# Optimization experiments

Hardware: AMD Instinct MI355X
Metric: run time of the kernel (lower is better)

## Reference

```python
import jax, jax.numpy as jnp
import numpy as np

B, L, D = 4, 512, 768          # batch, seq, d_model
NL, DI, N, K, R = 12, 1536, 16, 4, 48  # layers, d_inner, d_state, d_conv, dt_rank
V, P = 50257, 1024             # vocab, positions
EPS = 1e-5


def setup_inputs() -> dict:
    key = jax.random.key(0)
    ks = jax.random.split(key, 12)
    p = lambda i, shape, s=0.02: jax.random.normal(ks[i], shape, jnp.float32) * s
    return {
        "input_ids": jax.random.randint(ks[0], (B, L), 0, V),
        "wte": p(1, (V, D)),
        "wpe": p(2, (P, D)),
        "ln_g": jnp.ones((NL, D), jnp.float32),
        "ln_b": jnp.zeros((NL, D), jnp.float32),
        "in_W": p(3, (NL, 2 * DI, D)),
        "conv_W": p(4, (NL, DI, K), 0.2),
        "conv_b": jnp.zeros((NL, DI), jnp.float32),
        "xp_W": p(5, (NL, R + 2 * N, DI)),
        "dt_W": p(6, (NL, DI, R), 0.1),
        "dt_b": p(7, (NL, DI), 0.5),
        # Mamba S4D-real init: A = -exp(A_log), A_log = log(1..N)
        "A_log": jnp.tile(jnp.log(jnp.arange(1, N + 1, dtype=jnp.float32)), (NL, DI, 1)),
        "Dres": jnp.ones((NL, DI), jnp.float32),
        "out_W": p(8, (NL, D, DI)),
        "nf_g": jnp.ones((D,), jnp.float32),
        "nf_b": jnp.zeros((D,), jnp.float32),
        "fin_g": jnp.ones((D,), jnp.float32),
        "fin_b": jnp.zeros((D,), jnp.float32),
    }


def layer_norm(x, g, b):
    mu = jnp.mean(x, -1, keepdims=True)
    var = jnp.mean((x - mu) ** 2, -1, keepdims=True)
    return (x - mu) * jax.lax.rsqrt(var + EPS) * g + b


def causal_conv(x, w, b):
    # x: (B, L, DI); depthwise causal conv, kernel K, left pad K-1, truncate to L
    xt = jnp.transpose(x, (0, 2, 1))  # (B, DI, L)
    y = jax.lax.conv_general_dilated(
        xt, w[:, None, :], (1,), [(K - 1, 0)],
        feature_group_count=DI, dimension_numbers=("NCH", "OIH", "NCH"))
    return jnp.transpose(y + b[None, :, None], (0, 2, 1))


def selective_scan(u, delta, A, Bm, Cm):
    # u, delta: (B, L, DI); A: (DI, N); Bm, Cm: (B, L, N)
    def step(h, inp):
        u_t, d_t, b_t, c_t = inp  # (B,DI), (B,DI), (B,N), (B,N)
        dA = jnp.exp(d_t[:, :, None] * A)            # (B, DI, N)
        h = h * dA + (d_t * u_t)[:, :, None] * b_t[:, None, :]
        y = jnp.einsum("bdn,bn->bd", h, c_t)
        return h, y

    h0 = jnp.zeros((u.shape[0], DI, N), u.dtype)
    xs = (jnp.swapaxes(u, 0, 1), jnp.swapaxes(delta, 0, 1),
          jnp.swapaxes(Bm, 0, 1), jnp.swapaxes(Cm, 0, 1))
    _, ys = jax.lax.scan(step, h0, xs)               # ys: (L, B, DI)
    return jnp.swapaxes(ys, 0, 1)


def mamba_mixer(x, inW, cW, cb, xpW, dtW, dtb, a_log, dres, outW):
    xz = jnp.einsum("bld,ed->ble", x, inW)           # (B, L, 2*DI)
    xi, z = jnp.split(xz, 2, axis=-1)
    xi = jax.nn.silu(causal_conv(xi, cW, cb))
    dbl = jnp.einsum("bld,ed->ble", xi, xpW)         # (B, L, R+2N)
    dt, Bm, Cm = dbl[..., :R], dbl[..., R:R + N], dbl[..., R + N:]
    delta = jax.nn.softplus(jnp.einsum("blr,dr->bld", dt, dtW) + dtb)
    A = -jnp.exp(a_log)
    y = selective_scan(xi, delta, A, Bm, Cm) + xi * dres
    y = y * jax.nn.silu(z)
    return jnp.einsum("ble,de->bld", y, outW)


def reference(input_ids, wte, wpe, ln_g, ln_b, in_W, conv_W, conv_b, xp_W,
              dt_W, dt_b, A_log, Dres, out_W, nf_g, nf_b, fin_g, fin_b):
    emb = wte[input_ids] + wpe[: input_ids.shape[1]]  # (B, L, D); dropout=identity (eval)
    hidden, residual = emb, None
    for i in range(NL):
        residual = hidden if residual is None else hidden + residual
        h = layer_norm(residual, ln_g[i], ln_b[i])
        hidden = mamba_mixer(h, in_W[i], conv_W[i], conv_b[i], xp_W[i],
                             dt_W[i], dt_b[i], A_log[i], Dres[i], out_W[i])
    residual = hidden + residual
    out = layer_norm(residual, nf_g, nf_b)   # MixerModel.norm_f
    return layer_norm(out, fin_g, fin_b)     # decoder self.norm
```

## Files before the change

### kernel.cpp

```cpp
#include <hip/hip_runtime.h>

#define BB 4
#define LL 512
#define DD 768
#define NLAYER 12
#define DI 1536
#define NS 16
#define KC 4
#define RR 48
#define MROWS (BB*LL)
#define E2 (2*DI)
#define EPSV 1e-5f
#define CH2 16
#define LC2 (LL/CH2)
#define LOG2E 1.4426950408889634f
#define XPZ 12

typedef __attribute__((ext_vector_type(8))) short bf16x8;
typedef __attribute__((ext_vector_type(4))) float f32x4;

#define GLL16(g, l) __builtin_amdgcn_global_load_lds( \
    (const __attribute__((address_space(1))) void*)(g), \
    (__attribute__((address_space(3))) void*)(l), 16, 0, 0)

__device__ inline float hw_exp2(float x) { return __builtin_amdgcn_exp2f(x); }

__device__ inline ushort f2bf(float f) {
  union { float f; unsigned u; } v; v.f = f;
  unsigned u = v.u;
  unsigned r = (u + 0x7fffu + ((u >> 16) & 1u)) >> 16;
  return (ushort)r;
}
__device__ inline float bf2f(ushort u) {
  union { unsigned u; float f; } v; v.u = ((unsigned)u) << 16; return v.f;
}

__device__ inline float block_sum(float v, volatile float* red) {
  #pragma unroll
  for (int o = 32; o > 0; o >>= 1) v += __shfl_down(v, o);
  if ((threadIdx.x & 63) == 0) red[threadIdx.x >> 6] = v;
  __syncthreads();
  float t = red[0] + red[1] + red[2] + red[3];
  __syncthreads();
  return t;
}

__global__ __launch_bounds__(256) void k_cvtA(const float* __restrict__ inW,
    const float* __restrict__ outW, ushort* __restrict__ wIn,
    ushort* __restrict__ wOut) {
  int i = blockIdx.x * 256 + threadIdx.x;
  const int nIn = NLAYER * E2 * DD / 4;
  const int nOut = NLAYER * DD * DI / 4;
  if (i < nIn) {
    float4 v = ((const float4*)inW)[i];
    ushort4 o = { f2bf(v.x), f2bf(v.y), f2bf(v.z), f2bf(v.w) };
    ((ushort4*)wIn)[i] = o;
  } else if (i < nIn + nOut) {
    int j = i - nIn;
    float4 v = ((const float4*)outW)[j];
    ushort4 o = { f2bf(v.x), f2bf(v.y), f2bf(v.z), f2bf(v.w) };
    ((ushort4*)wOut)[j] = o;
  }
}

__global__ __launch_bounds__(256) void k_cvtB(const float* __restrict__ xpW,
    const float* __restrict__ dtW, const float* __restrict__ convW,
    ushort* __restrict__ wXp, ushort* __restrict__ wDt, float* __restrict__ convWt) {
  int i = blockIdx.x * 256 + threadIdx.x;
  const int n0 = NLAYER * 80 * DI / 4;
  const int n1 = NLAYER * DI * 64;
  const int n2 = NLAYER * DI * 4;
  if (i < n0) {
    float4 v = ((const float4*)xpW)[i];
    ushort4 o = { f2bf(v.x), f2bf(v.y), f2bf(v.z), f2bf(v.w) };
    ((ushort4*)wXp)[i] = o;
  } else if (i < n0 + n1) {
    int j = i - n0;
    int r = j >> 6, c = j & 63;
    wDt[j] = (c < RR) ? f2bf(dtW[(size_t)r * RR + c]) : (ushort)0;
  } else if (i < n0 + n1 + n2) {
    int j = i - n0 - n1;
    int l = j / (DI * 4);
    int rem = j - l * (DI * 4);
    int d = rem >> 2, k = rem & 3;
    convWt[(size_t)l * 4 * DI + k * DI + d] = convW[(size_t)l * DI * 4 + d * 4 + k];
  }
}

__global__ __launch_bounds__(256) void k_embed(const int* __restrict__ ids,
    const float* __restrict__ wte, const float* __restrict__ wpe,
    float* __restrict__ resid) {
  const int nd4 = DD / 4;
  int i = blockIdx.x * 256 + threadIdx.x;
  if (i >= MROWS * nd4) return;
  int m = i / nd4, d4 = i - m * nd4;
  int l = m & (LL - 1);
  int tok = ids[m];
  float4 a = ((const float4*)wte)[(size_t)tok * nd4 + d4];
  float4 b = ((const float4*)wpe)[(size_t)l * nd4 + d4];
  float4 o; o.x = a.x + b.x; o.y = a.y + b.y; o.z = a.z + b.z; o.w = a.w + b.w;
  ((float4*)resid)[i] = o;
}

__global__ __launch_bounds__(256) void k_ln(const float* __restrict__ h0,
    const float* __restrict__ h1,
    float* __restrict__ resid, const float* __restrict__ g, const float* __restrict__ b,
    ushort* __restrict__ hbf, int addHidden) {
  __shared__ float red[4];
  int m = blockIdx.x, t = threadIdx.x;
  size_t base = (size_t)m * DD;
  float x0 = resid[base + t], x1 = resid[base + t + 256], x2 = resid[base + t + 512];
  if (addHidden) {
    x0 += h0[base + t]       + h1[base + t];
    x1 += h0[base + t + 256] + h1[base + t + 256];
    x2 += h0[base + t + 512] + h1[base + t + 512];
    resid[base + t] = x0; resid[base + t + 256] = x1; resid[base + t + 512] = x2;
  }
  float S  = block_sum(x0 + x1 + x2, red);
  float S2 = block_sum(x0*x0 + x1*x1 + x2*x2, red);
  float mu = S * (1.f / DD);
  float var = S2 * (1.f / DD) - mu * mu;
  float rs = rsqrtf(var + EPSV);
  hbf[base + t]       = f2bf((x0 - mu) * rs * g[t]       + b[t]);
  hbf[base + t + 256] = f2bf((x1 - mu) * rs * g[t + 256] + b[t + 256]);
  hbf[base + t + 512] = f2bf((x2 - mu) * rs * g[t + 512] + b[t + 512]);
}

template<int OM>
__global__ __launch_bounds__(256) void k_gemm64(const ushort* __restrict__ A,
    const ushort* __restrict__ Bw, void* __restrict__ Cv, const float* __restrict__ dtb,
    int N, int K, int kSteps) {
  __shared__ ushort lA[64 * 64];
  __shared__ ushort lB[128 * 64];
  int tid = threadIdx.x;
  int wid = tid >> 6, lane = tid & 63;
  int tm = blockIdx.y * 64, tn = blockIdx.x * 128;
  int kBase = blockIdx.z * kSteps * 64;
  int wr = (wid >> 1) * 32, wc = (wid & 1) * 64;
  int fr = lane & 15, kg = lane >> 4;
  int sR = lane >> 3;
  int sC = ((lane & 7) ^ sR) * 8;
  f32x4 acc[2][4];
  #pragma unroll
  for (int mi = 0; mi < 2; ++mi)
    #pragma unroll
    for (int ni = 0; ni < 4; ++ni)
      acc[mi][ni] = {0.f, 0.f, 0.f, 0.f};

  for (int ks = 0; ks < kSteps; ++ks) {
    int k0 = kBase + ks * 64;
    #pragma unroll
    for (int i = 0; i < 2; ++i) {
      int r0 = wid * 16 + i * 8;
      GLL16(A + (size_t)(tm + r0 + sR) * K + k0 + sC, &lA[r0 * 64]);
    }
    #pragma unroll
    for (int i = 0; i < 4; ++i) {
      int r0 = wid * 32 + i * 8;
      int brow = tn + r0 + sR;
      if (brow > N - 1) brow = N - 1;
      GLL16(Bw + (size_t)brow * K + k0 + sC, &lB[r0 * 64]);
    }
    __syncthreads();
    #pragma unroll
    for (int k2 = 0; k2 < 2; ++k2) {
      bf16x8 af[2], bfr[4];
      #pragma unroll
      for (int mi = 0; mi < 2; ++mi)
        af[mi] = *(const bf16x8*)&lA[(wr + mi * 16 + fr) * 64 + (((k2 * 4 + kg) ^ (fr & 7)) * 8)];
      #pragma unroll
      for (int ni = 0; ni < 4; ++ni)
        bfr[ni] = *(const bf16x8*)&lB[(wc + ni * 16 + fr) * 64 + (((k2 * 4 + kg) ^ (fr & 7)) * 8)];
      #pragma unroll
      for (int mi = 0; mi < 2; ++mi)
        #pragma unroll
        for (int ni = 0; ni < 4; ++ni)
          acc[mi][ni] = __builtin_amdgcn_mfma_f32_16x16x32_bf16(af[mi], bfr[ni], acc[mi][ni], 0, 0, 0);
    }
    __syncthreads();
  }
  int crow0 = tm + wr + kg * 4;
  int ccol0 = tn + wc + fr;
  if (OM == 0) {
    float* C = (float*)Cv + (size_t)blockIdx.z * ((size_t)gridDim.y * 64) * N;
    #pragma unroll
    for (int mi = 0; mi < 2; ++mi)
      #pragma unroll
      for (int ni = 0; ni < 4; ++ni) {
        int cc = ccol0 + ni * 16;
        if (cc < N) {
          #pragma unroll
          for (int j = 0; j < 4; ++j)
            C[(size_t)(crow0 + mi * 16 + j) * N + cc] = acc[mi][ni][j];
        }
      }
  } else if (OM == 1) {
    ushort* C = (ushort*)Cv;
    #pragma unroll
    for (int mi = 0; mi < 2; ++mi)
      #pragma unroll
      for (int ni = 0; ni < 4; ++ni) {
        int cc = ccol0 + ni * 16;
        if (cc < N) {
          #pragma unroll
          for (int j = 0; j < 4; ++j)
            C[(size_t)(crow0 + mi * 16 + j) * N + cc] = f2bf(acc[mi][ni][j]);
        }
      }
  } else {
    float* C = (float*)Cv;
    #pragma unroll
    for (int mi = 0; mi < 2; ++mi)
      #pragma unroll
      for (int ni = 0; ni < 4; ++ni) {
        int cc = ccol0 + ni * 16;
        if (cc < N) {
          float bv = dtb[cc];
          #pragma unroll
          for (int j = 0; j < 4; ++j) {
            float x = acc[mi][ni][j] + bv;
            float sp = (x > 20.f) ? x : log1pf(__expf(x));
            C[(size_t)(crow0 + mi * 16 + j) * N + cc] = sp;
          }
        }
      }
  }
}

__global__ __launch_bounds__(256) void k_xpconv(const ushort* __restrict__ xz,
    const ushort* __restrict__ wXpL, const float* __restrict__ cwt,
    const float* __restrict__ cbl, ushort* __restrict__ xibf,
    float* __restrict__ xpPart) {
  __shared__ ushort lA[64 * 64];
  __shared__ ushort lB[128 * 64];
  int tid = threadIdx.x;
  int wid = tid >> 6, lane = tid & 63;
  int tm2 = blockIdx.y * 64;
  int kBase = blockIdx.z * 128;
  int wr = (wid >> 1) * 32, wc = (wid & 1) * 64;
  int fr = lane & 15, kg = lane >> 4;
  int sR = lane >> 3, sC = ((lane & 7) ^ sR) * 8;
  f32x4 acc[2][4];
  #pragma unroll
  for (int mi = 0; mi < 2; ++mi)
    #pragma unroll
    for (int ni = 0; ni < 4; ++ni)
      acc[mi][ni] = {0.f, 0.f, 0.f, 0.f};
  for (int ks = 0; ks < 2; ++ks) {
    int k0 = kBase + ks * 64;
    #pragma unroll
    for (int i2 = 0; i2 < 4; ++i2) {
      int r0 = wid * 32 + i2 * 8;
      int brow = r0 + sR;
      if (brow > 79) brow = 79;
      GLL16(wXpL + (size_t)brow * DI + k0 + sC, &lB[r0 * 64]);
    }
    #pragma unroll
    for (int c2 = 0; c2 < 2; ++c2) {
      int chunk = tid + c2 * 256;
      int row = chunk >> 3, cc8 = chunk & 7;
      int m = tm2 + row, l = m & (LL - 1);
      int gc = k0 + cc8 * 8;
      float a8[8];
      {
        float4 a = *(const float4*)&cbl[gc];
        float4 b = *(const float4*)&cbl[gc + 4];
        a8[0] = a.x; a8[1] = a.y; a8[2] = a.z; a8[3] = a.w;
        a8[4] = b.x; a8[5] = b.y; a8[6] = b.z; a8[7] = b.w;
      }
      #pragma unroll
      for (int t = 0; t < 4; ++t) {
        if (l - 3 + t >= 0) {
          float4 a = *(const float4*)&cwt[t * DI + gc];
          float4 b = *(const float4*)&cwt[t * DI + gc + 4];
          bf16x8 v = *(const bf16x8*)&xz[(size_t)(m - 3 + t) * E2 + gc];
          a8[0] += bf2f((ushort)v[0]) * a.x; a8[1] += bf2f((ushort)v[1]) * a.y;
          a8[2] += bf2f((ushort)v[2]) * a.z; a8[3] += bf2f((ushort)v[3]) * a.w;
          a8[4] += bf2f((ushort)v[4]) * b.x; a8[5] += bf2f((ushort)v[5]) * b.y;
          a8[6] += bf2f((ushort)v[6]) * b.z; a8[7] += bf2f((ushort)v[7]) * b.w;
        }
      }
      bf16x8 vo;
      #pragma unroll
      for (int j = 0; j < 8; ++j) {
        float sg = 1.f / (1.f + __expf(-a8[j]));
        vo[j] = (short)f2bf(a8[j] * sg);
      }
      *(bf16x8*)&lA[row * 64 + ((cc8 ^ (row & 7)) * 8)] = vo;
      *(bf16x8*)&xibf[(size_t)m * DI + gc] = vo;
    }
    __syncthreads();
    #pragma unroll
    for (int k2 = 0; k2 < 2; ++k2) {
      bf16x8 af[2], bf4[4];
      #pragma unroll
      for (int mi = 0; mi < 2; ++mi)
        af[mi] = *(const bf16x8*)&lA[(wr + mi * 16 + fr) * 64 + (((k2 * 4 + kg) ^ (fr & 7)) * 8)];
      #pragma unroll
      for (int ni = 0; ni < 4; ++ni)
        bf4[ni] = *(const bf16x8*)&lB[(wc + ni * 16 + fr) * 64 + (((k2 * 4 + kg) ^ (fr & 7)) * 8)];
      #pragma unroll
      for (int mi = 0; mi < 2; ++mi)
        #pragma unroll
        for (int ni = 0; ni < 4; ++ni)
          acc[mi][ni] = __builtin_amdgcn_mfma_f32_16x16x32_bf16(af[mi], bf4[ni], acc[mi][ni], 0, 0, 0);
    }
    __syncthreads();
  }
  int crow0 = tm2 + wr + kg * 4;
  int ccol0 = wc + fr;
  float* Cf = xpPart + (size_t)blockIdx.z * MROWS * 80;
  #pragma unroll
  for (int mi = 0; mi < 2; ++mi)
    #pragma unroll
    for (int ni = 0; ni < 4; ++ni) {
      int cc = ccol0 + ni * 16;
      if (cc < 80) {
        #pragma unroll
        for (int j = 0; j < 4; ++j)
          Cf[(size_t)(crow0 + mi * 16 + j) * 80 + cc] = acc[mi][ni][j];
      }
    }
}

__global__ __launch_bounds__(256) void k_comb_xp(const float* __restrict__ part,
    float* __restrict__ dblb, ushort* __restrict__ dtbf) {
  int i = blockIdx.x * 256 + threadIdx.x;
  if (i >= MROWS * 80) return;
  const int S = MROWS * 80;
  float s = 0.f;
  #pragma unroll
  for (int z = 0; z < XPZ; ++z) s += part[i + z * S];
  dblb[i] = s;
  int m = i / 80, c = i - m * 80;
  if (c < RR) dtbf[(size_t)m * 64 + c] = f2bf(s);
  else if (c < 64) dtbf[(size_t)m * 64 + c] = 0;
}

__global__ __launch_bounds__(256) void k_scan_f(const float* __restrict__ delta,
    const ushort* __restrict__ ubf, const float* __restrict__ dblb,
    const ushort* __restrict__ xz, const float* __restrict__ A_log,
    const float* __restrict__ Dres, ushort* __restrict__ ybf, int layer) {
  __shared__ float shH[16 * 257];
  __shared__ float shP[16 * 257];
  int tid = threadIdx.x;
  int dloc = tid & 15, chunk = tid >> 4;
  int d = blockIdx.x * 16 + dloc;
  int b = blockIdx.y;
  float an[16];
  {
    const float4* a4 = (const float4*)(A_log + ((size_t)layer * DI + d) * NS);
    #pragma unroll
    for (int q = 0; q < 4; ++q) {
      float4 v = a4[q];
      an[4*q]   = -__expf(v.x) * LOG2E; an[4*q+1] = -__expf(v.y) * LOG2E;
      an[4*q+2] = -__expf(v.z) * LOG2E; an[4*q+3] = -__expf(v.w) * LOG2E;
    }
  }
  int l0 = chunk * LC2;
  size_t rowd0 = ((size_t)b * LL + l0) * DI + d;
  size_t rowb0 = ((size_t)b * LL + l0) * 80 + RR;

  float h[16], pr[16];
  #pragma unroll
  for (int n = 0; n < 16; ++n) { h[n] = 0.f; pr[n] = 1.f; }
  {
    size_t rd = rowd0, rb = rowb0;
    float dl = delta[rd];
    float uv = bf2f(ubf[rd]);
    float4 b0 = *(const float4*)(dblb + rb),     b1 = *(const float4*)(dblb + rb + 4);
    float4 b2 = *(const float4*)(dblb + rb + 8), b3 = *(const float4*)(dblb + rb + 12);
    for (int l = 0; l < LC2; ++l) {
      float dlc = dl, uvc = uv;
      float4 c0 = b0, c1 = b1, c2 = b2, c3 = b3;
      if (l + 1 < LC2) {
        rd += DI; rb += 80;
        dl = delta[rd]; uv = bf2f(ubf[rd]);
        b0 = *(const float4*)(dblb + rb);     b1 = *(const float4*)(dblb + rb + 4);
        b2 = *(const float4*)(dblb + rb + 8); b3 = *(const float4*)(dblb + rb + 12);
      }
      float du = dlc * uvc;
      float Bv[16] = { c0.x, c0.y, c0.z, c0.w, c1.x, c1.y, c1.z, c1.w,
                       c2.x, c2.y, c2.z, c2.w, c3.x, c3.y, c3.z, c3.w };
      #pragma unroll
      for (int n = 0; n < 16; ++n) {
        float a = hw_exp2(dlc * an[n]);
        h[n] = h[n] * a + du * Bv[n];
        pr[n] *= a;
      }
    }
  }
  {
    int base = dloc * 257 + chunk * 16;
    #pragma unroll
    for (int n = 0; n < 16; ++n) { shH[base + n] = h[n]; shP[base + n] = pr[n]; }
  }
  __syncthreads();
  {
    int n2 = tid & 15, dl2 = tid >> 4;
    float hh = 0.f;
    int base = dl2 * 257;
    for (int c = 0; c < CH2; ++c) {
      int idx = base + c * 16 + n2;
      float t = shH[idx], p = shP[idx];
      shH[idx] = hh;
      hh = t + p * hh;
    }
  }
  __syncthreads();
  {
    int base = dloc * 257 + chunk * 16;
    #pragma unroll
    for (int n = 0; n < 16; ++n) h[n] = shH[base + n];
  }
  float dresv = Dres[(size_t)layer * DI + d];
  {
    size_t rd = rowd0, rb = rowb0;
    size_t rz = ((size_t)b * LL + l0) * E2 + DI + d;
    float dl = delta[rd];
    float uv = bf2f(ubf[rd]);
    float4 b0 = *(const float4*)(dblb + rb),      b1 = *(const float4*)(dblb + rb + 4);
    float4 b2 = *(const float4*)(dblb + rb + 8),  b3 = *(const float4*)(dblb + rb + 12);
    float4 e0 = *(const float4*)(dblb + rb + 16), e1 = *(const float4*)(dblb + rb + 20);
    float4 e2 = *(const float4*)(dblb + rb + 24), e3 = *(const float4*)(dblb + rb + 28);
    for (int l = 0; l < LC2; ++l) {
      float dlc = dl, uvc = uv;
      float4 c0 = b0, c1 = b1, c2 = b2, c3 = b3;
      float4 f0 = e0, f1 = e1, f2 = e2, f3 = e3;
      size_t rdc = rd, rzc = rz;
      if (l + 1 < LC2) {
        rd += DI; rb += 80; rz += E2;
        dl = delta[rd]; uv = bf2f(ubf[rd]);
        b0 = *(const float4*)(dblb + rb);      b1 = *(const float4*)(dblb + rb + 4);
        b2 = *(const float4*)(dblb + rb + 8);  b3 = *(const float4*)(dblb + rb + 12);
        e0 = *(const float4*)(dblb + rb + 16); e1 = *(const float4*)(dblb + rb + 20);
        e2 = *(const float4*)(dblb + rb + 24); e3 = *(const float4*)(dblb + rb + 28);
      }
      float du = dlc * uvc;
      float Bv[16] = { c0.x, c0.y, c0.z, c0.w, c1.x, c1.y, c1.z, c1.w,
                       c2.x, c2.y, c2.z, c2.w, c3.x, c3.y, c3.z, c3.w };
      float Cv[16] = { f0.x, f0.y, f0.z, f0.w, f1.x, f1.y, f1.z, f1.w,
                       f2.x, f2.y, f2.z, f2.w, f3.x, f3.y, f3.z, f3.w };
      float y = 0.f;
      #pragma unroll
      for (int n = 0; n < 16; ++n) {
        float a = hw_exp2(dlc * an[n]);
        h[n] = h[n] * a + du * Bv[n];
        y += h[n] * Cv[n];
      }
      float zv = bf2f(xz[rzc]);
      float yt = y + uvc * dresv;
      float sg = 1.f / (1.f + __expf(-zv));
      ybf[rdc] = f2bf(yt * (zv * sg));
    }
  }
}

__global__ __launch_bounds__(256) void k_final(const float* __restrict__ resid,
    const float* __restrict__ h0, const float* __restrict__ h1,
    const float* __restrict__ nfg, const float* __restrict__ nfb,
    const float* __restrict__ fig, const float* __restrict__ fib,
    float* __restrict__ out) {
  __shared__ float red[4];
  int m = blockIdx.x, t = threadIdx.x;
  size_t base = (size_t)m * DD;
  float x0 = resid[base + t]       + h0[base + t]       + h1[base + t];
  float x1 = resid[base + t + 256] + h0[base + t + 256] + h1[base + t + 256];
  float x2 = resid[base + t + 512] + h0[base + t + 512] + h1[base + t + 512];
  float S  = block_sum(x0 + x1 + x2, red);
  float S2 = block_sum(x0*x0 + x1*x1 + x2*x2, red);
  float mu = S * (1.f / DD);
  float var = S2 * (1.f / DD) - mu * mu;
  float rs = rsqrtf(var + EPSV);
  float t0 = (x0 - mu) * rs * nfg[t]       + nfb[t];
  float t1 = (x1 - mu) * rs * nfg[t + 256] + nfb[t + 256];
  float t2 = (x2 - mu) * rs * nfg[t + 512] + nfb[t + 512];
  S  = block_sum(t0 + t1 + t2, red);
  S2 = block_sum(t0*t0 + t1*t1 + t2*t2, red);
  mu = S * (1.f / DD);
  var = S2 * (1.f / DD) - mu * mu;
  rs = rsqrtf(var + EPSV);
  out[base + t]       = (t0 - mu) * rs * fig[t]       + fib[t];
  out[base + t + 256] = (t1 - mu) * rs * fig[t + 256] + fib[t + 256];
  out[base + t + 512] = (t2 - mu) * rs * fig[t + 512] + fib[t + 512];
}

extern "C" void kernel_launch(void* const* d_in, const int* in_sizes, int n_in,
                              void* d_out, int out_size, void* d_ws, size_t ws_size,
                              hipStream_t stream) {
  const int*   ids    = (const int*)  d_in[0];
  const float* wte    = (const float*)d_in[1];
  const float* wpe    = (const float*)d_in[2];
  const float* ln_g   = (const float*)d_in[3];
  const float* ln_b   = (const float*)d_in[4];
  const float* in_W   = (const float*)d_in[5];
  const float* conv_W = (const float*)d_in[6];
  const float* conv_b = (const float*)d_in[7];
  const float* xp_W   = (const float*)d_in[8];
  const float* dt_W   = (const float*)d_in[9];
  const float* dt_b   = (const float*)d_in[10];
  const float* A_log  = (const float*)d_in[11];
  const float* Dres   = (const float*)d_in[12];
  const float* out_W  = (const float*)d_in[13];
  const float* nf_g   = (const float*)d_in[14];
  const float* nf_b   = (const float*)d_in[15];
  const float* fin_g  = (const float*)d_in[16];
  const float* fin_b  = (const float*)d_in[17];

  char* p = (char*)d_ws;
  auto take = [&](size_t bytes) {
    char* r = p; p += (bytes + 255) & ~(size_t)255; return r;
  };
  float*  resid  = (float*) take((size_t)MROWS * DD * 4);
  float*  hidP   = (float*) take((size_t)2 * MROWS * DD * 4);
  ushort* h_bf   = (ushort*)take((size_t)MROWS * DD * 2);
  ushort* xz     = (ushort*)take((size_t)MROWS * E2 * 2);
  ushort* xibf   = (ushort*)take((size_t)MROWS * DI * 2);
  float*  xpPart = (float*) take((size_t)XPZ * MROWS * 80 * 4);
  float*  dblb   = (float*) take((size_t)MROWS * 80 * 4);
  ushort* dtbf   = (ushort*)take((size_t)MROWS * 64 * 2);
  float*  delta  = (float*) take((size_t)MROWS * DI * 4);
  ushort* ybf    = (ushort*)take((size_t)MROWS * DI * 2);
  ushort* wInBf  = (ushort*)take((size_t)NLAYER * E2 * DD * 2);
  ushort* wXpBf  = (ushort*)take((size_t)NLAYER * 80 * DI * 2);
  ushort* wDtBf  = (ushort*)take((size_t)NLAYER * DI * 64 * 2);
  ushort* wOutBf = (ushort*)take((size_t)NLAYER * DD * DI * 2);
  float*  convWt = (float*) take((size_t)NLAYER * 4 * DI * 4);

  {
    int total = NLAYER * E2 * DD / 4 + NLAYER * DD * DI / 4;
    k_cvtA<<<(total + 255) / 256, 256, 0, stream>>>(in_W, out_W, wInBf, wOutBf);
  }
  {
    int total = NLAYER * 80 * DI / 4 + NLAYER * DI * 64 + NLAYER * DI * 4;
    k_cvtB<<<(total + 255) / 256, 256, 0, stream>>>(xp_W, dt_W, conv_W,
                                                    wXpBf, wDtBf, convWt);
  }
  k_embed<<<(MROWS * (DD / 4) + 255) / 256, 256, 0, stream>>>(ids, wte, wpe, resid);

  for (int i = 0; i < NLAYER; ++i) {
    k_ln<<<MROWS, 256, 0, stream>>>(hidP, hidP + (size_t)MROWS * DD, resid,
                                    ln_g + (size_t)i * DD, ln_b + (size_t)i * DD,
                                    h_bf, i > 0 ? 1 : 0);

    { dim3 g(E2 / 128, MROWS / 64, 1);
      k_gemm64<1><<<g, 256, 0, stream>>>(h_bf, wInBf + (size_t)i * E2 * DD,
                                         (void*)xz, nullptr, E2, DD, DD / 64); }

    { dim3 g(1, MROWS / 64, XPZ);
      k_xpconv<<<g, 256, 0, stream>>>(xz, wXpBf + (size_t)i * 80 * DI,
                                      convWt + (size_t)i * 4 * DI,
                                      conv_b + (size_t)i * DI, xibf, xpPart); }

    k_comb_xp<<<(MROWS * 80 + 255) / 256, 256, 0, stream>>>(xpPart, dblb, dtbf);

    { dim3 g(DI / 128, MROWS / 64, 1);
      k_gemm64<2><<<g, 256, 0, stream>>>(dtbf, wDtBf + (size_t)i * DI * 64,
                                         (void*)delta, dt_b + (size_t)i * DI, DI, 64, 1); }

    { dim3 g(DI / 16, BB);
      k_scan_f<<<g, 256, 0, stream>>>(delta, xibf, dblb, xz, A_log, Dres, ybf, i); }

    { dim3 g(DD / 128, MROWS / 64, 2);
      k_gemm64<0><<<g, 256, 0, stream>>>(ybf, wOutBf + (size_t)i * DD * DI,
                                         (void*)hidP, nullptr, DD, DI, DI / 64 / 2); }
  }

  k_final<<<MROWS, 256, 0, stream>>>(resid, hidP, hidP + (size_t)MROWS * DD,
                                     nf_g, nf_b, fin_g, fin_b, (float*)d_out);
}
```

Measured before the change: 1.349 ms.

## Widen parallelism in scan, xp, dt and out-projection kernels

The selective scan now uses 32 chunks of 16 steps with 8 channels per block, so it launches more blocks and runs shorter serial chains. The per-chunk decay product is computed in closed form as exp2(A·sum(delta)) instead of a running product. The x-projection split-K doubles to 24 slices of 64, the dt GEMM uses 64-wide N tiles, and the out-projection splits K four ways. All of this raises occupancy on a GPU with many CUs, at the cost of larger partial buffers, more reduction traffic in the layer-norm and combine steps, and a longer combine pass across chunks.

```diff
diff --git a/kernel.cpp b/kernel.cpp
--- a/kernel.cpp
+++ b/kernel.cpp
@@ -11,10 +11,13 @@
 #define MROWS (BB*LL)
 #define E2 (2*DI)
 #define EPSV 1e-5f
-#define CH2 16
-#define LC2 (LL/CH2)
 #define LOG2E 1.4426950408889634f
-#define XPZ 12
+#define XPZ 24
+#define OZ 4
+#define SCH 32
+#define SLC (LL/SCH)
+#define SDL 8
+#define SSTR (SCH*16 + 5)
 
 typedef __attribute__((ext_vector_type(8))) short bf16x8;
 typedef __attribute__((ext_vector_type(4))) float f32x4;
@@ -102,8 +105,7 @@
   ((float4*)resid)[i] = o;
 }
 
-__global__ __launch_bounds__(256) void k_ln(const float* __restrict__ h0,
-    const float* __restrict__ h1,
+__global__ __launch_bounds__(256) void k_ln(const float* __restrict__ hidP,
     float* __restrict__ resid, const float* __restrict__ g, const float* __restrict__ b,
     ushort* __restrict__ hbf, int addHidden) {
   __shared__ float red[4];
@@ -111,9 +113,11 @@
   size_t base = (size_t)m * DD;
   float x0 = resid[base + t], x1 = resid[base + t + 256], x2 = resid[base + t + 512];
   if (addHidden) {
-    x0 += h0[base + t]       + h1[base + t];
-    x1 += h0[base + t + 256] + h1[base + t + 256];
-    x2 += h0[base + t + 512] + h1[base + t + 512];
+    #pragma unroll
+    for (int z = 0; z < OZ; ++z) {
+      size_t bz = (size_t)z * MROWS * DD + base;
+      x0 += hidP[bz + t]; x1 += hidP[bz + t + 256]; x2 += hidP[bz + t + 512];
+    }
     resid[base + t] = x0; resid[base + t + 256] = x1; resid[base + t + 512] = x2;
   }
   float S  = block_sum(x0 + x1 + x2, red);
@@ -126,25 +130,26 @@
   hbf[base + t + 512] = f2bf((x2 - mu) * rs * g[t + 512] + b[t + 512]);
 }
 
-template<int OM>
+template<int OM, int NT>
 __global__ __launch_bounds__(256) void k_gemm64(const ushort* __restrict__ A,
     const ushort* __restrict__ Bw, void* __restrict__ Cv, const float* __restrict__ dtb,
     int N, int K, int kSteps) {
+  constexpr int NR = NT / 32;
   __shared__ ushort lA[64 * 64];
-  __shared__ ushort lB[128 * 64];
+  __shared__ ushort lB[NT * 64];
   int tid = threadIdx.x;
   int wid = tid >> 6, lane = tid & 63;
-  int tm = blockIdx.y * 64, tn = blockIdx.x * 128;
+  int tm = blockIdx.y * 64, tn = blockIdx.x * NT;
   int kBase = blockIdx.z * kSteps * 64;
-  int wr = (wid >> 1) * 32, wc = (wid & 1) * 64;
+  int wr = (wid >> 1) * 32, wc = (wid & 1) * (NT / 2);
   int fr = lane & 15, kg = lane >> 4;
   int sR = lane >> 3;
   int sC = ((lane & 7) ^ sR) * 8;
-  f32x4 acc[2][4];
+  f32x4 acc[2][NR];
   #pragma unroll
   for (int mi = 0; mi < 2; ++mi)
     #pragma unroll
-    for (int ni = 0; ni < 4; ++ni)
+    for (int ni = 0; ni < NR; ++ni)
       acc[mi][ni] = {0.f, 0.f, 0.f, 0.f};
 
   for (int ks = 0; ks < kSteps; ++ks) {
@@ -155,8 +160,8 @@
       GLL16(A + (size_t)(tm + r0 + sR) * K + k0 + sC, &lA[r0 * 64]);
     }
     #pragma unroll
-    for (int i = 0; i < 4; ++i) {
-      int r0 = wid * 32 + i * 8;
+    for (int i = 0; i < NR; ++i) {
+      int r0 = wid * (NT / 4) + i * 8;
       int brow = tn + r0 + sR;
       if (brow > N - 1) brow = N - 1;
       GLL16(Bw + (size_t)brow * K + k0 + sC, &lB[r0 * 64]);
@@ -164,17 +169,17 @@
     __syncthreads();
     #pragma unroll
     for (int k2 = 0; k2 < 2; ++k2) {
-      bf16x8 af[2], bfr[4];
+      bf16x8 af[2], bfr[NR];
       #pragma unroll
       for (int mi = 0; mi < 2; ++mi)
         af[mi] = *(const bf16x8*)&lA[(wr + mi * 16 + fr) * 64 + (((k2 * 4 + kg) ^ (fr & 7)) * 8)];
       #pragma unroll
-      for (int ni = 0; ni < 4; ++ni)
+      for (int ni = 0; ni < NR; ++ni)
         bfr[ni] = *(const bf16x8*)&lB[(wc + ni * 16 + fr) * 64 + (((k2 * 4 + kg) ^ (fr & 7)) * 8)];
       #pragma unroll
       for (int mi = 0; mi < 2; ++mi)
         #pragma unroll
-        for (int ni = 0; ni < 4; ++ni)
+        for (int ni = 0; ni < NR; ++ni)
           acc[mi][ni] = __builtin_amdgcn_mfma_f32_16x16x32_bf16(af[mi], bfr[ni], acc[mi][ni], 0, 0, 0);
     }
     __syncthreads();
@@ -186,7 +191,7 @@
     #pragma unroll
     for (int mi = 0; mi < 2; ++mi)
       #pragma unroll
-      for (int ni = 0; ni < 4; ++ni) {
+      for (int ni = 0; ni < NR; ++ni) {
         int cc = ccol0 + ni * 16;
         if (cc < N) {
           #pragma unroll
@@ -199,7 +204,7 @@
     #pragma unroll
     for (int mi = 0; mi < 2; ++mi)
       #pragma unroll
-      for (int ni = 0; ni < 4; ++ni) {
+      for (int ni = 0; ni < NR; ++ni) {
         int cc = ccol0 + ni * 16;
         if (cc < N) {
           #pragma unroll
@@ -212,7 +217,7 @@
     #pragma unroll
     for (int mi = 0; mi < 2; ++mi)
       #pragma unroll
-      for (int ni = 0; ni < 4; ++ni) {
+      for (int ni = 0; ni < NR; ++ni) {
         int cc = ccol0 + ni * 16;
         if (cc < N) {
           float bv = dtb[cc];
@@ -236,7 +241,7 @@
   int tid = threadIdx.x;
   int wid = tid >> 6, lane = tid & 63;
   int tm2 = blockIdx.y * 64;
-  int kBase = blockIdx.z * 128;
+  int k0 = blockIdx.z * 64;
   int wr = (wid >> 1) * 32, wc = (wid & 1) * 64;
   int fr = lane & 15, kg = lane >> 4;
   int sR = lane >> 3, sC = ((lane & 7) ^ sR) * 8;
@@ -246,67 +251,64 @@
     #pragma unroll
     for (int ni = 0; ni < 4; ++ni)
       acc[mi][ni] = {0.f, 0.f, 0.f, 0.f};
-  for (int ks = 0; ks < 2; ++ks) {
-    int k0 = kBase + ks * 64;
-    #pragma unroll
-    for (int i2 = 0; i2 < 4; ++i2) {
-      int r0 = wid * 32 + i2 * 8;
-      int brow = r0 + sR;
-      if (brow > 79) brow = 79;
-      GLL16(wXpL + (size_t)brow * DI + k0 + sC, &lB[r0 * 64]);
-    }
-    #pragma unroll
-    for (int c2 = 0; c2 < 2; ++c2) {
-      int chunk = tid + c2 * 256;
-      int row = chunk >> 3, cc8 = chunk & 7;
-      int m = tm2 + row, l = m & (LL - 1);
-      int gc = k0 + cc8 * 8;
-      float a8[8];
-      {
-        float4 a = *(const float4*)&cbl[gc];
-        float4 b = *(const float4*)&cbl[gc + 4];
-        a8[0] = a.x; a8[1] = a.y; a8[2] = a.z; a8[3] = a.w;
-        a8[4] = b.x; a8[5] = b.y; a8[6] = b.z; a8[7] = b.w;
-      }
-      #pragma unroll
-      for (int t = 0; t < 4; ++t) {
-        if (l - 3 + t >= 0) {
-          float4 a = *(const float4*)&cwt[t * DI + gc];
-          float4 b = *(const float4*)&cwt[t * DI + gc + 4];
-          bf16x8 v = *(const bf16x8*)&xz[(size_t)(m - 3 + t) * E2 + gc];
-          a8[0] += bf2f((ushort)v[0]) * a.x; a8[1] += bf2f((ushort)v[1]) * a.y;
-          a8[2] += bf2f((ushort)v[2]) * a.z; a8[3] += bf2f((ushort)v[3]) * a.w;
-          a8[4] += bf2f((ushort)v[4]) * b.x; a8[5] += bf2f((ushort)v[5]) * b.y;
-          a8[6] += bf2f((ushort)v[6]) * b.z; a8[7] += bf2f((ushort)v[7]) * b.w;
-        }
-      }
-      bf16x8 vo;
-      #pragma unroll
-      for (int j = 0; j < 8; ++j) {
-        float sg = 1.f / (1.f + __expf(-a8[j]));
-        vo[j] = (short)f2bf(a8[j] * sg);
-      }
-      *(bf16x8*)&lA[row * 64 + ((cc8 ^ (row & 7)) * 8)] = vo;
-      *(bf16x8*)&xibf[(size_t)m * DI + gc] = vo;
-    }
-    __syncthreads();
-    #pragma unroll
-    for (int k2 = 0; k2 < 2; ++k2) {
-      bf16x8 af[2], bf4[4];
-      #pragma unroll
-      for (int mi = 0; mi < 2; ++mi)
-        af[mi] = *(const bf16x8*)&lA[(wr + mi * 16 + fr) * 64 + (((k2 * 4 + kg) ^ (fr & 7)) * 8)];
+  #pragma unroll
+  for (int i2 = 0; i2 < 4; ++i2) {
+    int r0 = wid * 32 + i2 * 8;
+    int brow = r0 + sR;
+    if (brow > 79) brow = 79;
+    GLL16(wXpL + (size_t)brow * DI + k0 + sC, &lB[r0 * 64]);
+  }
+  #pragma unroll
+  for (int c2 = 0; c2 < 2; ++c2) {
+    int chunk = tid + c2 * 256;
+    int row = chunk >> 3, cc8 = chunk & 7;
+    int m = tm2 + row, l = m & (LL - 1);
+    int gc = k0 + cc8 * 8;
+    float a8[8];
+    {
+      float4 a = *(const float4*)&cbl[gc];
+      float4 b = *(const float4*)&cbl[gc + 4];
+      a8[0] = a.x; a8[1] = a.y; a8[2] = a.z; a8[3] = a.w;
+      a8[4] = b.x; a8[5] = b.y; a8[6] = b.z; a8[7] = b.w;
+    }
+    #pragma unroll
+    for (int t = 0; t < 4; ++t) {
+      if (l - 3 + t >= 0) {
+        float4 a = *(const float4*)&cwt[t * DI + gc];
+        float4 b = *(const float4*)&cwt[t * DI + gc + 4];
+        bf16x8 v = *(const bf16x8*)&xz[(size_t)(m - 3 + t) * E2 + gc];
+        a8[0] += bf2f((ushort)v[0]) * a.x; a8[1] += bf2f((ushort)v[1]) * a.y;
+        a8[2] += bf2f((ushort)v[2]) * a.z; a8[3] += bf2f((ushort)v[3]) * a.w;
+        a8[4] += bf2f((ushort)v[4]) * b.x; a8[5] += bf2f((ushort)v[5]) * b.y;
+        a8[6] += bf2f((ushort)v[6]) * b.z; a8[7] += bf2f((ushort)v[7]) * b.w;
+      }
+    }
+    bf16x8 vo;
+    #pragma unroll
+    for (int j = 0; j < 8; ++j) {
+      float sg = 1.f / (1.f + __expf(-a8[j]));
+      vo[j] = (short)f2bf(a8[j] * sg);
+    }
+    *(bf16x8*)&lA[row * 64 + ((cc8 ^ (row & 7)) * 8)] = vo;
+    *(bf16x8*)&xibf[(size_t)m * DI + gc] = vo;
+  }
+  __syncthreads();
+  #pragma unroll
+  for (int k2 = 0; k2 < 2; ++k2) {
+    bf16x8 af[2], bf4[4];
+    #pragma unroll
+    for (int mi = 0; mi < 2; ++mi)
+      af[mi] = *(const bf16x8*)&lA[(wr + mi * 16 + fr) * 64 + (((k2 * 4 + kg) ^ (fr & 7)) * 8)];
+    #pragma unroll
+    for (int ni = 0; ni < 4; ++ni)
+      bf4[ni] = *(const bf16x8*)&lB[(wc + ni * 16 + fr) * 64 + (((k2 * 4 + kg) ^ (fr & 7)) * 8)];
+    #pragma unroll
+    for (int mi = 0; mi < 2; ++mi)
       #pragma unroll
       for (int ni = 0; ni < 4; ++ni)
-        bf4[ni] = *(const bf16x8*)&lB[(wc + ni * 16 + fr) * 64 + (((k2 * 4 + kg) ^ (fr & 7)) * 8)];
-      #pragma unroll
-      for (int mi = 0; mi < 2; ++mi)
-        #pragma unroll
-        for (int ni = 0; ni < 4; ++ni)
-          acc[mi][ni] = __builtin_amdgcn_mfma_f32_16x16x32_bf16(af[mi], bf4[ni], acc[mi][ni], 0, 0, 0);
-    }
-    __syncthreads();
-  }
+        acc[mi][ni] = __builtin_amdgcn_mfma_f32_16x16x32_bf16(af[mi], bf4[ni], acc[mi][ni], 0, 0, 0);
+  }
+  __syncthreads();
   int crow0 = tm2 + wr + kg * 4;
   int ccol0 = wc + fr;
   float* Cf = xpPart + (size_t)blockIdx.z * MROWS * 80;
@@ -341,11 +343,11 @@
     const ushort* __restrict__ ubf, const float* __restrict__ dblb,
     const ushort* __restrict__ xz, const float* __restrict__ A_log,
     const float* __restrict__ Dres, ushort* __restrict__ ybf, int layer) {
-  __shared__ float shH[16 * 257];
-  __shared__ float shP[16 * 257];
+  __shared__ float shH[SDL * SSTR];
+  __shared__ float shP[SDL * SSTR];
   int tid = threadIdx.x;
-  int dloc = tid & 15, chunk = tid >> 4;
-  int d = blockIdx.x * 16 + dloc;
+  int dloc = tid & (SDL - 1), chunk = tid >> 3;
+  int d = blockIdx.x * SDL + dloc;
   int b = blockIdx.y;
   float an[16];
   {
@@ -357,50 +359,55 @@
       an[4*q+2] = -__expf(v.z) * LOG2E; an[4*q+3] = -__expf(v.w) * LOG2E;
     }
   }
-  int l0 = chunk * LC2;
+  int l0 = chunk * SLC;
   size_t rowd0 = ((size_t)b * LL + l0) * DI + d;
   size_t rowb0 = ((size_t)b * LL + l0) * 80 + RR;
 
-  float h[16], pr[16];
-  #pragma unroll
-  for (int n = 0; n < 16; ++n) { h[n] = 0.f; pr[n] = 1.f; }
+  float h[16];
+  float sumD = 0.f;
+  #pragma unroll
+  for (int n = 0; n < 16; ++n) h[n] = 0.f;
   {
     size_t rd = rowd0, rb = rowb0;
     float dl = delta[rd];
     float uv = bf2f(ubf[rd]);
     float4 b0 = *(const float4*)(dblb + rb),     b1 = *(const float4*)(dblb + rb + 4);
     float4 b2 = *(const float4*)(dblb + rb + 8), b3 = *(const float4*)(dblb + rb + 12);
-    for (int l = 0; l < LC2; ++l) {
+    for (int l = 0; l < SLC; ++l) {
       float dlc = dl, uvc = uv;
       float4 c0 = b0, c1 = b1, c2 = b2, c3 = b3;
-      if (l + 1 < LC2) {
+      if (l + 1 < SLC) {
         rd += DI; rb += 80;
         dl = delta[rd]; uv = bf2f(ubf[rd]);
         b0 = *(const float4*)(dblb + rb);     b1 = *(const float4*)(dblb + rb + 4);
         b2 = *(const float4*)(dblb + rb + 8); b3 = *(const float4*)(dblb + rb + 12);
       }
       float du = dlc * uvc;
+      sumD += dlc;
       float Bv[16] = { c0.x, c0.y, c0.z, c0.w, c1.x, c1.y, c1.z, c1.w,
                        c2.x, c2.y, c2.z, c2.w, c3.x, c3.y, c3.z, c3.w };
       #pragma unroll
       for (int n = 0; n < 16; ++n) {
         float a = hw_exp2(dlc * an[n]);
         h[n] = h[n] * a + du * Bv[n];
-        pr[n] *= a;
-      }
-    }
-  }
-  {
-    int base = dloc * 257 + chunk * 16;
-    #pragma unroll
-    for (int n = 0; n < 16; ++n) { shH[base + n] = h[n]; shP[base + n] = pr[n]; }
+      }
+    }
+  }
+  {
+    int base = dloc * SSTR + chunk * 16;
+    #pragma unroll
+    for (int n = 0; n < 16; ++n) {
+      shH[base + n] = h[n];
+      shP[base + n] = hw_exp2(an[n] * sumD);
+    }
   }
   __syncthreads();
-  {
+
+  if (tid < SDL * 16) {
     int n2 = tid & 15, dl2 = tid >> 4;
     float hh = 0.f;
-    int base = dl2 * 257;
-    for (int c = 0; c < CH2; ++c) {
+    int base = dl2 * SSTR;
+    for (int c = 0; c < SCH; ++c) {
       int idx = base + c * 16 + n2;
       float t = shH[idx], p = shP[idx];
       shH[idx] = hh;
@@ -408,8 +415,9 @@
     }
   }
   __syncthreads();
-  {
-    int base = dloc * 257 + chunk * 16;
+
+  {
+    int base = dloc * SSTR + chunk * 16;
     #pragma unroll
     for (int n = 0; n < 16; ++n) h[n] = shH[base + n];
   }
@@ -423,12 +431,12 @@
     float4 b2 = *(const float4*)(dblb + rb + 8),  b3 = *(const float4*)(dblb + rb + 12);
     float4 e0 = *(const float4*)(dblb + rb + 16), e1 = *(const float4*)(dblb + rb + 20);
     float4 e2 = *(const float4*)(dblb + rb + 24), e3 = *(const float4*)(dblb + rb + 28);
-    for (int l = 0; l < LC2; ++l) {
+    for (int l = 0; l < SLC; ++l) {
       float dlc = dl, uvc = uv;
       float4 c0 = b0, c1 = b1, c2 = b2, c3 = b3;
       float4 f0 = e0, f1 = e1, f2 = e2, f3 = e3;
       size_t rdc = rd, rzc = rz;
-      if (l + 1 < LC2) {
+      if (l + 1 < SLC) {
         rd += DI; rb += 80; rz += E2;
         dl = delta[rd]; uv = bf2f(ubf[rd]);
         b0 = *(const float4*)(dblb + rb);      b1 = *(const float4*)(dblb + rb + 4);
@@ -457,16 +465,19 @@
 }
 
 __global__ __launch_bounds__(256) void k_final(const float* __restrict__ resid,
-    const float* __restrict__ h0, const float* __restrict__ h1,
+    const float* __restrict__ hidP,
     const float* __restrict__ nfg, const float* __restrict__ nfb,
     const float* __restrict__ fig, const float* __restrict__ fib,
     float* __restrict__ out) {
   __shared__ float red[4];
   int m = blockIdx.x, t = threadIdx.x;
   size_t base = (size_t)m * DD;
-  float x0 = resid[base + t]       + h0[base + t]       + h1[base + t];
-  float x1 = resid[base + t + 256] + h0[base + t + 256] + h1[base + t + 256];
-  float x2 = resid[base + t + 512] + h0[base + t + 512] + h1[base + t + 512];
+  float x0 = resid[base + t], x1 = resid[base + t + 256], x2 = resid[base + t + 512];
+  #pragma unroll
+  for (int z = 0; z < OZ; ++z) {
+    size_t bz = (size_t)z * MROWS * DD + base;
+    x0 += hidP[bz + t]; x1 += hidP[bz + t + 256]; x2 += hidP[bz + t + 512];
+  }
   float S  = block_sum(x0 + x1 + x2, red);
   float S2 = block_sum(x0*x0 + x1*x1 + x2*x2, red);
   float mu = S * (1.f / DD);
@@ -512,7 +523,7 @@
     char* r = p; p += (bytes + 255) & ~(size_t)255; return r;
   };
   float*  resid  = (float*) take((size_t)MROWS * DD * 4);
-  float*  hidP   = (float*) take((size_t)2 * MROWS * DD * 4);
+  float*  hidP   = (float*) take((size_t)OZ * MROWS * DD * 4);
   ushort* h_bf   = (ushort*)take((size_t)MROWS * DD * 2);
   ushort* xz     = (ushort*)take((size_t)MROWS * E2 * 2);
   ushort* xibf   = (ushort*)take((size_t)MROWS * DI * 2);
@@ -539,13 +550,13 @@
   k_embed<<<(MROWS * (DD / 4) + 255) / 256, 256, 0, stream>>>(ids, wte, wpe, resid);
 
   for (int i = 0; i < NLAYER; ++i) {
-    k_ln<<<MROWS, 256, 0, stream>>>(hidP, hidP + (size_t)MROWS * DD, resid,
+    k_ln<<<MROWS, 256, 0, stream>>>(hidP, resid,
                                     ln_g + (size_t)i * DD, ln_b + (size_t)i * DD,
                                     h_bf, i > 0 ? 1 : 0);
 
     { dim3 g(E2 / 128, MROWS / 64, 1);
-      k_gemm64<1><<<g, 256, 0, stream>>>(h_bf, wInBf + (size_t)i * E2 * DD,
-                                         (void*)xz, nullptr, E2, DD, DD / 64); }
+      k_gemm64<1, 128><<<g, 256, 0, stream>>>(h_bf, wInBf + (size_t)i * E2 * DD,
+                                              (void*)xz, nullptr, E2, DD, DD / 64); }
 
     { dim3 g(1, MROWS / 64, XPZ);
       k_xpconv<<<g, 256, 0, stream>>>(xz, wXpBf + (size_t)i * 80 * DI,
@@ -554,18 +565,18 @@
 
     k_comb_xp<<<(MROWS * 80 + 255) / 256, 256, 0, stream>>>(xpPart, dblb, dtbf);
 
-    { dim3 g(DI / 128, MROWS / 64, 1);
-      k_gemm64<2><<<g, 256, 0, stream>>>(dtbf, wDtBf + (size_t)i * DI * 64,
-                                         (void*)delta, dt_b + (size_t)i * DI, DI, 64, 1); }
-
-    { dim3 g(DI / 16, BB);
+    { dim3 g(DI / 64, MROWS / 64, 1);
+      k_gemm64<2, 64><<<g, 256, 0, stream>>>(dtbf, wDtBf + (size_t)i * DI * 64,
+                                             (void*)delta, dt_b + (size_t)i * DI, DI, 64, 1); }
+
+    { dim3 g(DI / SDL, BB);
       k_scan_f<<<g, 256, 0, stream>>>(delta, xibf, dblb, xz, A_log, Dres, ybf, i); }
 
-    { dim3 g(DD / 128, MROWS / 64, 2);
-      k_gemm64<0><<<g, 256, 0, stream>>>(ybf, wOutBf + (size_t)i * DD * DI,
-                                         (void*)hidP, nullptr, DD, DI, DI / 64 / 2); }
-  }
-
-  k_final<<<MROWS, 256, 0, stream>>>(resid, hidP, hidP + (size_t)MROWS * DD,
-                                     nf_g, nf_b, fin_g, fin_b, (float*)d_out);
-}
+    { dim3 g(DD / 128, MROWS / 64, OZ);
+      k_gemm64<0, 128><<<g, 256, 0, stream>>>(ybf, wOutBf + (size_t)i * DD * DI,
+                                              (void*)hidP, nullptr, DD, DI, DI / 64 / OZ); }
+  }
+
+  k_final<<<MROWS, 256, 0, stream>>>(resid, hidP, nf_g, nf_b,
+                                     fin_g, fin_b, (float*)d_out);
+}
```

Result: slower. 1.412 ms (+4.6%).
